# Optimization experiments

Hardware: AMD Instinct MI355X
Metric: run time of the kernel (lower is better)

The kernel has to match this reference:

```python
import jax, jax.numpy as jnp
import numpy as np

N_HEAD = 16
N_KV_HEAD = 4
D_HEAD = 128
RMS_EPS = 1.1920929e-07  # torch default eps for fp32 rms_norm


def _rms_norm(x):
    return x * jax.lax.rsqrt(jnp.mean(x * x, axis=-1, keepdims=True) + RMS_EPS)


def _rotary_tables(n_pos, dim):
    # dim = d_head; freq table has dim//2 entries (half of them zero)
    angular_freq = (1.0 / 1024.0) ** jnp.linspace(0.0, 1.0, dim // 4, dtype=jnp.float32)
    angular_freq = jnp.concatenate([angular_freq, jnp.zeros(dim // 4, jnp.float32)])
    theta = jnp.arange(n_pos, dtype=jnp.float32)[:, None] * angular_freq[None, :]
    return jnp.cos(theta), jnp.sin(theta)


def _apply_rotary(x):
    # x: (B, H, T, D). Faithful to source: cos/sin indexed by x.shape[-3] (= H),
    # broadcast over the time axis.
    n = x.shape[-3]
    cos, sin = _rotary_tables(n, x.shape[-1])
    cos = cos[None, :, None, :]
    sin = sin[None, :, None, :]
    xf = x.astype(jnp.float32)
    x1, x2 = jnp.split(xf, 2, axis=-1)
    y1 = x1 * cos + x2 * sin
    y2 = -x1 * sin + x2 * cos
    return jnp.concatenate([y1, y2], axis=-1).astype(x.dtype)


def setup_inputs() -> dict:
    key = jax.random.key(0)
    k1, k2, k3, k4 = jax.random.split(key, 4)
    B, T, C = 2, 2048, 2048
    return {
        "x": jax.random.normal(k1, (B, T, C), jnp.float32),
        "Wq": jax.random.normal(k2, (C, C), jnp.float32) * 0.02,
        "Wkv": jax.random.normal(k3, (2 * N_KV_HEAD * D_HEAD, C), jnp.float32) * 0.02,
        "Wproj": jax.random.normal(k4, (C, C), jnp.float32) * 0.02,
        "tok_masks": jnp.ones((B, T), jnp.int32),
    }


def reference(x, Wq, Wkv, Wproj, tok_masks):
    B, T, C = x.shape
    nh, nkv, dh = N_HEAD, N_KV_HEAD, D_HEAD

    q = (x @ Wq.T).reshape(B, T, nh, dh).transpose(0, 2, 1, 3)          # (B,nh,T,dh)
    kv = x @ Wkv.T                                                       # (B,T,2*nkv*dh)
    k, v = jnp.split(kv, 2, axis=2)
    k = k.reshape(B, T, nkv, dh).transpose(0, 2, 1, 3)                   # (B,nkv,T,dh)
    v = v.reshape(B, T, nkv, dh).transpose(0, 2, 1, 3)

    q, k = _rms_norm(q), _rms_norm(k)
    q, k = _apply_rotary(q), _apply_rotary(k)

    # GQA: repeat kv heads to match query heads
    rep = nh // nkv
    k = jnp.repeat(k, rep, axis=1)
    v = jnp.repeat(v, rep, axis=1)

    scale = 1.0 / jnp.sqrt(jnp.float32(dh))
    scores = jnp.einsum("bhqd,bhkd->bhqk", q, k) * scale                 # (B,nh,T,T)
    causal = jnp.tril(jnp.ones((T, T), bool))
    scores = jnp.where(causal[None, None], scores, -jnp.inf)
    attn = jax.nn.softmax(scores, axis=-1)
    y = jnp.einsum("bhqk,bhkd->bhqd", attn, v)                           # (B,nh,T,dh)
    y = y.transpose(0, 2, 1, 3).reshape(B, T, C)
    y = y @ Wproj.T
    return (y, jnp.float32(0.0))
```

## Files before the change

kernel.cpp:

```cpp
#include <hip/hip_runtime.h>
#include <hip/hip_bf16.h>

#define T_SEQ 2048
#define BATCH 2
#define CDIM  2048
#define NH    16
#define NKV   4
#define DH    128

typedef __attribute__((ext_vector_type(8))) short bfrag;
typedef __attribute__((ext_vector_type(4))) short bhalf;
typedef __attribute__((ext_vector_type(4))) float ffrag;
typedef __hip_bfloat16 bf16;

__device__ __forceinline__ void gll16(const bf16* __restrict__ g, bf16* lds) {
    __builtin_amdgcn_global_load_lds((const __attribute__((address_space(1))) void*)g,
                                     (__attribute__((address_space(3))) void*)lds, 16, 0, 0);
}

__device__ __forceinline__ unsigned cvt_pk_bf16(float lo, float hi) {
    unsigned r;
    asm("v_cvt_pk_bf16_f32 %0, %1, %2" : "=v"(r) : "v"(lo), "v"(hi));
    return r;
}

struct bf16x4 { bf16 a, b, c, d; };
#define N4_X   (BATCH * T_SEQ * CDIM / 4)
#define N4_WQ  (CDIM * CDIM / 4)
#define N4_WKV (2 * NKV * DH * CDIM / 4)
#define N4_WP  (CDIM * CDIM / 4)
__global__ __launch_bounds__(256) void cast_all(
    const float* __restrict__ x, const float* __restrict__ wq,
    const float* __restrict__ wkv, const float* __restrict__ wp,
    bf16* __restrict__ xb, bf16* __restrict__ wqb, bf16* __restrict__ wkvb, bf16* __restrict__ wpb)
{
    int j = blockIdx.x * 256 + threadIdx.x;
    const float* s; bf16* d;
    if (j < N4_X) { s = x; d = xb; }
    else {
        j -= N4_X;
        if (j < N4_WQ) { s = wq; d = wqb; }
        else {
            j -= N4_WQ;
            if (j < N4_WKV) { s = wkv; d = wkvb; }
            else { j -= N4_WKV; if (j >= N4_WP) return; s = wp; d = wpb; }
        }
    }
    float4 f = ((const float4*)s)[j];
    bf16x4 o{__float2bfloat16(f.x), __float2bfloat16(f.y),
             __float2bfloat16(f.z), __float2bfloat16(f.w)};
    ((bf16x4*)d)[j] = o;
}

template<int MODE, int BN>
__device__ __forceinline__ void gemm_body(
    const bf16* __restrict__ A, const bf16* __restrict__ W, int m0, int n0,
    bf16* __restrict__ out0, bf16* __restrict__ out1, float* __restrict__ outf,
    bf16* __restrict__ sA, bf16* __restrict__ sB)
{
    constexpr int NG = BN / 32;

    const int lane = threadIdx.x & 63;
    const int w    = threadIdx.x >> 6;
    const int wm   = w >> 1, wn = w & 1;
    const int lr   = lane & 15, quad = lane >> 4;

    const int pr8  = lane >> 3;
    const int ls   = (lane & 7) ^ pr8;
    const int rloc = 2 * (w * 8 + pr8) + (ls >> 2);
    const int k0s  = (ls & 3) * 8;

    const bf16* Aj0 = A + (size_t)(m0 +      rloc) * CDIM + k0s;
    const bf16* Aj1 = A + (size_t)(m0 + 64 + rloc) * CDIM + k0s;
    const bf16* Bj0 = W + (size_t)(n0 +      rloc) * CDIM + k0s;
    const bf16* Bj1 = W + (size_t)(n0 + 64 + rloc) * CDIM + k0s;
    bf16* dA0 = sA +        w * 512;
    bf16* dA1 = sA + 2048 + w * 512;
    bf16* dB0 = sB +        w * 512;
    bf16* dB1 = sB + 2048 + w * 512;

    const int soff = ((((lr & 1) << 2) | quad) ^ ((lr >> 1) & 7)) << 3;

    ffrag acc[4][NG] = {};
    for (int kk = 0; kk < CDIM; kk += 32) {
        __syncthreads();
        gll16(Aj0 + kk, dA0);
        gll16(Aj1 + kk, dA1);
        gll16(Bj0 + kk, dB0);
        if constexpr (BN == 128) gll16(Bj1 + kk, dB1);
        __syncthreads();

        bfrag af[4], bg[NG];
        #pragma unroll
        for (int f = 0; f < 4; ++f)
            af[f] = *(const bfrag*)&sA[((f * 16 + wm * 8 + (lr >> 1)) << 6) + soff];
        #pragma unroll
        for (int g = 0; g < NG; ++g)
            bg[g] = *(const bfrag*)&sB[((g * 16 + wn * 8 + (lr >> 1)) << 6) + soff];
        #pragma unroll
        for (int f = 0; f < 4; ++f)
            #pragma unroll
            for (int g = 0; g < NG; ++g)
                acc[f][g] = __builtin_amdgcn_mfma_f32_16x16x32_bf16(af[f], bg[g], acc[f][g], 0, 0, 0);
    }

    #pragma unroll
    for (int f = 0; f < 4; ++f) {
        #pragma unroll
        for (int g = 0; g < NG; ++g) {
            #pragma unroll
            for (int i = 0; i < 4; ++i) {
                const int m = m0 + f * 32 + wm * 16 + quad * 4 + i;
                const int n = n0 + g * 32 + wn * 16 + lr;
                const float v = acc[f][g][i];
                if constexpr (MODE == 0) {
                    int b = m >> 11, t = m & (T_SEQ - 1);
                    int h = n >> 7, d = n & (DH - 1);
                    out0[(((size_t)(b * NH + h) * T_SEQ + t) << 7) + d] = __float2bfloat16(v);
                } else if constexpr (MODE == 1) {
                    int b = m >> 11, t = m & (T_SEQ - 1);
                    if (n < NKV * DH) {
                        int h = n >> 7, d = n & (DH - 1);
                        out0[(((size_t)(b * NKV + h) * T_SEQ + t) << 7) + d] = __float2bfloat16(v);
                    } else {
                        int n2 = n - NKV * DH;
                        int h = n2 >> 7, d = n2 & (DH - 1);
                        out1[(((size_t)(b * NKV + h) * DH + d) << 11) + t] = __float2bfloat16(v);
                    }
                } else {
                    outf[(size_t)m * CDIM + n] = v;
                }
            }
        }
    }
}

__global__ __launch_bounds__(256) void gemm_qkv(
    const bf16* __restrict__ A, const bf16* __restrict__ Wq, const bf16* __restrict__ Wkv,
    bf16* __restrict__ q, bf16* __restrict__ k, bf16* __restrict__ vt)
{
    __shared__ __align__(16) bf16 sA[64 * 64];
    __shared__ __align__(16) bf16 sB[64 * 64];
    if (blockIdx.y < 16)
        gemm_body<0, 128>(A, Wq, blockIdx.x * 128, blockIdx.y * 128, q, nullptr, nullptr, sA, sB);
    else
        gemm_body<1, 128>(A, Wkv, blockIdx.x * 128, (blockIdx.y - 16) * 128, k, vt, nullptr, sA, sB);
}

__global__ __launch_bounds__(256) void gemm_proj(
    const bf16* __restrict__ A, const bf16* __restrict__ W, float* __restrict__ outf)
{
    __shared__ __align__(16) bf16 sA[64 * 64];
    __shared__ __align__(16) bf16 sB[32 * 64];
    gemm_body<2, 64>(A, W, blockIdx.x * 128, blockIdx.y * 64, nullptr, nullptr, outf, sA, sB);
    if (blockIdx.x == 0 && blockIdx.y == 0 && threadIdx.x == 0)
        outf[(size_t)BATCH * T_SEQ * CDIM] = 0.0f;
}

#define QROWS (BATCH * NH * T_SEQ)
#define KROWS (BATCH * NKV * T_SEQ)
__global__ __launch_bounds__(256) void normrope_k(bf16* __restrict__ qb, bf16* __restrict__ kb) {
    int row = blockIdx.x * 4 + (threadIdx.x >> 6);
    bf16* bufb; int nheads;
    if (row < QROWS) { bufb = qb; nheads = NH; }
    else { row -= QROWS; bufb = kb; nheads = NKV; }
    const int h = (row >> 11) % nheads;
    bf16* p = bufb + (size_t)row * DH;
    const int d = threadIdx.x & 63;
    float x1 = __bfloat162float(p[d]);
    float x2 = __bfloat162float(p[d + 64]);
    float ss = x1 * x1 + x2 * x2;
    #pragma unroll
    for (int off = 32; off; off >>= 1) ss += __shfl_xor(ss, off);
    float r = rsqrtf(ss * (1.0f / 128.0f) + 1.1920929e-07f);
    x1 *= r; x2 *= r;
    float freq = (d < 32) ? exp2f(-10.0f * (float)d * (1.0f / 31.0f)) : 0.0f;
    float th = (float)h * freq;
    float c, s;
    __sincosf(th, &s, &c);
    p[d]      = __float2bfloat16(x1 * c + x2 * s);
    p[d + 64] = __float2bfloat16(-x1 * s + x2 * c);
}

__global__ __launch_bounds__(512, 2) void attn_k(const bf16* __restrict__ Q, const bf16* __restrict__ K,
                                                 const bf16* __restrict__ VT, bf16* __restrict__ Y)
{
    const int lane = threadIdx.x & 63;
    const int w = threadIdx.x >> 6;
    const int g = w >> 2, wl = w & 3;
    const int h = blockIdx.y, b = blockIdx.z;
    const int lr = lane & 15, quad = lane >> 4, lk = quad * 8;
    const bf16* Qb = Q  + (size_t)(b * NH  + h)        * T_SEQ * DH;
    const bf16* Kb = K  + (size_t)(b * NKV + (h >> 2)) * T_SEQ * DH;
    const bf16* Vb = VT + (size_t)(b * NKV + (h >> 2)) * DH * T_SEQ;

    __shared__ __align__(16) union ShmU {
        struct { bf16 SK[2][2][32 * 128]; bf16 SV[2][2][128 * 32]; } s;
        ffrag MRG[9 * 4 * 64];
    } shm;

    const int k_r0 = wl * 8 + (lane >> 4);
    const int k_ch = lane & 15;
    const int v_r0 = wl * 32 + (lane >> 2);
    const int v_ch = lane & 3;
    const int vsw = (lr + (lr >> 2)) & 3;
    const float scale = 0.08838834764831845f;

    auto load_v_perm = [&](const bf16* rp) {
        union { bhalf h[2]; bfrag f; } u;
        u.h[0] = *(const bhalf*)(rp + v_ch * 4);
        u.h[1] = *(const bhalf*)(rp + 16 + v_ch * 4);
        return u.f;
    };

    const int qb = 15 - blockIdx.x;
    const int nc = 2 * (qb + 1);
    const int q0 = qb * 128 + wl * 32;

    bfrag qf[2][4];
    #pragma unroll
    for (int t = 0; t < 2; ++t)
        #pragma unroll
        for (int dc = 0; dc < 4; ++dc)
            qf[t][dc] = *(const bfrag*)(Qb + (size_t)(q0 + t * 16 + lr) * DH + dc * 32 + lk);

    float lp[2] = {};
    ffrag o[2][8] = {};

    bfrag kr[2], vr[2];
    {
        const int b0 = g * 32;
        #pragma unroll
        for (int j = 0; j < 2; ++j) {
            kr[j] = *(const bfrag*)(Kb + (size_t)(b0 + k_r0 + j * 4) * DH + k_ch * 8);
            vr[j] = load_v_perm(Vb + (size_t)(v_r0 + j * 16) * T_SEQ + b0);
        }
        #pragma unroll
        for (int j = 0; j < 2; ++j) {
            int krow = k_r0 + j * 4;
            *(bfrag*)&shm.s.SK[g][0][krow * 128 + ((k_ch ^ (krow & 15))) * 8] = kr[j];
            int vrow = v_r0 + j * 16;
            *(bfrag*)&shm.s.SV[g][0][vrow * 32 + ((v_ch ^ ((vrow + (vrow >> 2)) & 3))) * 8] = vr[j];
        }
        if (nc > 1) {
            const int nb = 64 + g * 32;
            #pragma unroll
            for (int j = 0; j < 2; ++j) {
                kr[j] = *(const bfrag*)(Kb + (size_t)(nb + k_r0 + j * 4) * DH + k_ch * 8);
                vr[j] = load_v_perm(Vb + (size_t)(v_r0 + j * 16) * T_SEQ + nb);
            }
        }
    }
    __syncthreads();

    for (int c = 0; c < nc; ++c) {
        const int cur = c & 1, nxt = cur ^ 1;
        const int base = c * 64 + g * 32;
        const bf16* SKc = shm.s.SK[g][cur];
        const bf16* SVc = shm.s.SV[g][cur];

        if (c + 1 < nc) {
            #pragma unroll
            for (int j = 0; j < 2; ++j) {
                int krow = k_r0 + j * 4;
                *(bfrag*)&shm.s.SK[g][nxt][krow * 128 + ((k_ch ^ (krow & 15))) * 8] = kr[j];
                int vrow = v_r0 + j * 16;
                *(bfrag*)&shm.s.SV[g][nxt][vrow * 32 + ((v_ch ^ ((vrow + (vrow >> 2)) & 3))) * 8] = vr[j];
            }
            if (c + 2 < nc) {
                const int nb = (c + 2) * 64 + g * 32;
                #pragma unroll
                for (int j = 0; j < 2; ++j) {
                    kr[j] = *(const bfrag*)(Kb + (size_t)(nb + k_r0 + j * 4) * DH + k_ch * 8);
                    vr[j] = load_v_perm(Vb + (size_t)(v_r0 + j * 16) * T_SEQ + nb);
                }
            }
        }

        ffrag s2[2][2] = {};
        #pragma unroll
        for (int kt = 0; kt < 2; ++kt)
            #pragma unroll
            for (int dc = 0; dc < 4; ++dc) {
                bfrag kf = *(const bfrag*)&SKc[(kt * 16 + lr) * 128 + (((dc << 2) | quad) ^ lr) * 8];
                s2[0][kt] = __builtin_amdgcn_mfma_f32_16x16x32_bf16(kf, qf[0][dc], s2[0][kt], 0, 0, 0);
                s2[1][kt] = __builtin_amdgcn_mfma_f32_16x16x32_bf16(kf, qf[1][dc], s2[1][kt], 0, 0, 0);
            }

        const bool maskc = (c >= 2 * qb);
        bfrag pf[2];
        #pragma unroll
        for (int t = 0; t < 2; ++t) {
            const int qa = q0 + t * 16 + lr;
            float ev[2][4];
            #pragma unroll
            for (int kt = 0; kt < 2; ++kt)
                #pragma unroll
                for (int i = 0; i < 4; ++i) {
                    const int ka = base + kt * 16 + quad * 4 + i;
                    float e = (!maskc || ka <= qa) ? __expf(fmaf(s2[t][kt][i], scale, -16.0f)) : 0.0f;
                    lp[t] += e;
                    ev[kt][i] = e;
                }
            union { unsigned u[4]; bfrag f; } pu;
            pu.u[0] = cvt_pk_bf16(ev[0][0], ev[0][1]);
            pu.u[1] = cvt_pk_bf16(ev[0][2], ev[0][3]);
            pu.u[2] = cvt_pk_bf16(ev[1][0], ev[1][1]);
            pu.u[3] = cvt_pk_bf16(ev[1][2], ev[1][3]);
            pf[t] = pu.f;
        }

        #pragma unroll
        for (int dt = 0; dt < 8; ++dt) {
            bfrag vf = *(const bfrag*)&SVc[(dt * 16 + lr) * 32 + ((quad ^ vsw)) * 8];
            o[0][dt] = __builtin_amdgcn_mfma_f32_16x16x32_bf16(pf[0], vf, o[0][dt], 0, 0, 0);
            o[1][dt] = __builtin_amdgcn_mfma_f32_16x16x32_bf16(pf[1], vf, o[1][dt], 0, 0, 0);
        }

        __syncthreads();
    }

    __syncthreads();
    #pragma unroll
    for (int t = 0; t < 2; ++t) {
        if (g == 1) {
            #pragma unroll
            for (int d = 0; d < 8; ++d) shm.MRG[(d * 4 + wl) * 64 + lane] = o[t][d];
            ffrag l4 = {lp[t], 0.0f, 0.0f, 0.0f};
            shm.MRG[(8 * 4 + wl) * 64 + lane] = l4;
        }
        __syncthreads();
        if (g == 0) {
            #pragma unroll
            for (int d = 0; d < 8; ++d) o[t][d] += shm.MRG[(d * 4 + wl) * 64 + lane];
            float lsum = lp[t] + shm.MRG[(8 * 4 + wl) * 64 + lane][0];
            lsum += __shfl_xor(lsum, 16);
            lsum += __shfl_xor(lsum, 32);
            float inv[4];
            #pragma unroll
            for (int i = 0; i < 4; ++i)
                inv[i] = 1.0f / __shfl(lsum, quad * 4 + i);
            #pragma unroll
            for (int dt = 0; dt < 8; ++dt)
                #pragma unroll
                for (int i = 0; i < 4; ++i) {
                    int row = q0 + t * 16 + quad * 4 + i;
                    Y[((size_t)(b * T_SEQ) + row) * CDIM + h * DH + dt * 16 + lr] =
                        __float2bfloat16(o[t][dt][i] * inv[i]);
                }
        }
        __syncthreads();
    }
}

extern "C" void kernel_launch(void* const* d_in, const int* in_sizes, int n_in,
                              void* d_out, int out_size, void* d_ws, size_t ws_size,
                              hipStream_t stream) {
    const float* x     = (const float*)d_in[0];
    const float* Wq    = (const float*)d_in[1];
    const float* Wkv   = (const float*)d_in[2];
    const float* Wproj = (const float*)d_in[3];
    float* out = (float*)d_out;

    char* ws = (char*)d_ws;
    size_t off = 0;
    auto alloc = [&](size_t bytes) { void* p = ws + off; off += (bytes + 255) & ~255ULL; return p; };
    bf16* xb   = (bf16*)alloc((size_t)BATCH * T_SEQ * CDIM * 2);
    bf16* wqb  = (bf16*)alloc((size_t)CDIM * CDIM * 2);
    bf16* wkvb = (bf16*)alloc((size_t)2 * NKV * DH * CDIM * 2);
    bf16* wpb  = (bf16*)alloc((size_t)CDIM * CDIM * 2);
    bf16* qb   = (bf16*)alloc((size_t)BATCH * NH * T_SEQ * DH * 2);
    bf16* kb   = (bf16*)alloc((size_t)BATCH * NKV * T_SEQ * DH * 2);
    bf16* vtb  = (bf16*)alloc((size_t)BATCH * NKV * DH * T_SEQ * 2);
    bf16* y1   = (bf16*)alloc((size_t)BATCH * T_SEQ * CDIM * 2);

    const int total4 = N4_X + N4_WQ + N4_WKV + N4_WP;
    cast_all<<<(total4 + 255) / 256, 256, 0, stream>>>(x, Wq, Wkv, Wproj, xb, wqb, wkvb, wpb);

    gemm_qkv<<<dim3(32, 24), 256, 0, stream>>>(xb, wqb, wkvb, qb, kb, vtb);
    normrope_k<<<(QROWS + KROWS) / 4, 256, 0, stream>>>(qb, kb);
    attn_k<<<dim3(16, NH, BATCH), 512, 0, stream>>>(qb, kb, vtb, y1);
    gemm_proj<<<dim3(32, 32), 256, 0, stream>>>(y1, wpb, out);
}
```

Baseline: 340.6 us.

## Restructure attention into 4-wave blocks with paired causal query tiles

The attention kernel goes from 512-thread blocks, where two wave groups split the key range and merge partial results through shared memory, to 256-thread blocks. Each wave now owns 16 query rows and sweeps all keys in 64-key chunks. Each block handles two query tiles (p and 15-p) in sequence so causal work is balanced across blocks. This removes the cross-group merge and its barriers, but halves the waves per block and makes each block's work serial over two passes.

```diff
diff --git a/kernel.cpp b/kernel.cpp
--- a/kernel.cpp
+++ b/kernel.cpp
@@ -182,174 +182,157 @@
     p[d + 64] = __float2bfloat16(-x1 * s + x2 * c);
 }
 
-__global__ __launch_bounds__(512, 2) void attn_k(const bf16* __restrict__ Q, const bf16* __restrict__ K,
+__global__ __launch_bounds__(256, 2) void attn_k(const bf16* __restrict__ Q, const bf16* __restrict__ K,
                                                  const bf16* __restrict__ VT, bf16* __restrict__ Y)
 {
     const int lane = threadIdx.x & 63;
     const int w = threadIdx.x >> 6;
-    const int g = w >> 2, wl = w & 3;
+    const int p = blockIdx.x >> 1, half = blockIdx.x & 1;
     const int h = blockIdx.y, b = blockIdx.z;
     const int lr = lane & 15, quad = lane >> 4, lk = quad * 8;
     const bf16* Qb = Q  + (size_t)(b * NH  + h)        * T_SEQ * DH;
     const bf16* Kb = K  + (size_t)(b * NKV + (h >> 2)) * T_SEQ * DH;
     const bf16* Vb = VT + (size_t)(b * NKV + (h >> 2)) * DH * T_SEQ;
 
-    __shared__ __align__(16) union ShmU {
-        struct { bf16 SK[2][2][32 * 128]; bf16 SV[2][2][128 * 32]; } s;
-        ffrag MRG[9 * 4 * 64];
-    } shm;
-
-    const int k_r0 = wl * 8 + (lane >> 4);
-    const int k_ch = lane & 15;
-    const int v_r0 = wl * 32 + (lane >> 2);
-    const int v_ch = lane & 3;
-    const int vsw = (lr + (lr >> 2)) & 3;
+    __shared__ __align__(16) bf16 SK[2][64 * 128];
+    __shared__ __align__(16) bf16 SV[2][128 * 64];
+
+    const int k_row = w * 16 + quad;
+    const int k_ch  = lane & 15;
+    const int v_row = w * 32 + (lane >> 3);
+    const int v_sl  = lane & 7;
+    const int vc    = v_sl ^ (lane >> 3);
+    const int vH    = vc >> 2, vs = vc & 3;
     const float scale = 0.08838834764831845f;
 
-    auto load_v_perm = [&](const bf16* rp) {
-        union { bhalf h[2]; bfrag f; } u;
-        u.h[0] = *(const bhalf*)(rp + v_ch * 4);
-        u.h[1] = *(const bhalf*)(rp + 16 + v_ch * 4);
+    auto load_v = [&](int kbase, int j) {
+        const bf16* rp = Vb + (size_t)(v_row + j * 8) * T_SEQ + kbase;
+        union { bhalf h2[2]; bfrag f; } u;
+        u.h2[0] = *(const bhalf*)(rp + vH * 32 + vs * 4);
+        u.h2[1] = *(const bhalf*)(rp + vH * 32 + 16 + vs * 4);
         return u.f;
     };
 
-    const int qb = 15 - blockIdx.x;
-    const int nc = 2 * (qb + 1);
-    const int q0 = qb * 128 + wl * 32;
-
-    bfrag qf[2][4];
-    #pragma unroll
-    for (int t = 0; t < 2; ++t)
+    for (int pass = 0; pass < 2; ++pass) {
+        const int qb = pass ? (15 - p) : p;
+        const int nc = 2 * (qb + 1);
+        const int q0w = qb * 128 + half * 64 + w * 16;
+
+        bfrag qf[4];
         #pragma unroll
         for (int dc = 0; dc < 4; ++dc)
-            qf[t][dc] = *(const bfrag*)(Qb + (size_t)(q0 + t * 16 + lr) * DH + dc * 32 + lk);
-
-    float lp[2] = {};
-    ffrag o[2][8] = {};
-
-    bfrag kr[2], vr[2];
-    {
-        const int b0 = g * 32;
-        #pragma unroll
-        for (int j = 0; j < 2; ++j) {
-            kr[j] = *(const bfrag*)(Kb + (size_t)(b0 + k_r0 + j * 4) * DH + k_ch * 8);
-            vr[j] = load_v_perm(Vb + (size_t)(v_r0 + j * 16) * T_SEQ + b0);
-        }
-        #pragma unroll
-        for (int j = 0; j < 2; ++j) {
-            int krow = k_r0 + j * 4;
-            *(bfrag*)&shm.s.SK[g][0][krow * 128 + ((k_ch ^ (krow & 15))) * 8] = kr[j];
-            int vrow = v_r0 + j * 16;
-            *(bfrag*)&shm.s.SV[g][0][vrow * 32 + ((v_ch ^ ((vrow + (vrow >> 2)) & 3))) * 8] = vr[j];
-        }
-        if (nc > 1) {
-            const int nb = 64 + g * 32;
-            #pragma unroll
-            for (int j = 0; j < 2; ++j) {
-                kr[j] = *(const bfrag*)(Kb + (size_t)(nb + k_r0 + j * 4) * DH + k_ch * 8);
-                vr[j] = load_v_perm(Vb + (size_t)(v_r0 + j * 16) * T_SEQ + nb);
-            }
-        }
-    }
-    __syncthreads();
-
-    for (int c = 0; c < nc; ++c) {
-        const int cur = c & 1, nxt = cur ^ 1;
-        const int base = c * 64 + g * 32;
-        const bf16* SKc = shm.s.SK[g][cur];
-        const bf16* SVc = shm.s.SV[g][cur];
-
-        if (c + 1 < nc) {
-            #pragma unroll
-            for (int j = 0; j < 2; ++j) {
-                int krow = k_r0 + j * 4;
-                *(bfrag*)&shm.s.SK[g][nxt][krow * 128 + ((k_ch ^ (krow & 15))) * 8] = kr[j];
-                int vrow = v_r0 + j * 16;
-                *(bfrag*)&shm.s.SV[g][nxt][vrow * 32 + ((v_ch ^ ((vrow + (vrow >> 2)) & 3))) * 8] = vr[j];
-            }
-            if (c + 2 < nc) {
-                const int nb = (c + 2) * 64 + g * 32;
+            qf[dc] = *(const bfrag*)(Qb + (size_t)(q0w + lr) * DH + dc * 32 + lk);
+
+        float lp = 0.0f;
+        ffrag o[8] = {};
+
+        bfrag kr[4], vr[4];
+        #pragma unroll
+        for (int j = 0; j < 4; ++j) {
+            kr[j] = *(const bfrag*)(Kb + (size_t)(k_row + j * 4) * DH + k_ch * 8);
+            vr[j] = load_v(0, j);
+        }
+        #pragma unroll
+        for (int j = 0; j < 4; ++j) {
+            int krow = k_row + j * 4;
+            *(bfrag*)&SK[0][krow * 128 + ((k_ch ^ (krow & 15)) << 3)] = kr[j];
+            int vrow = v_row + j * 8;
+            *(bfrag*)&SV[0][vrow * 64 + (v_sl << 3)] = vr[j];
+        }
+        #pragma unroll
+        for (int j = 0; j < 4; ++j) {
+            kr[j] = *(const bfrag*)(Kb + (size_t)(64 + k_row + j * 4) * DH + k_ch * 8);
+            vr[j] = load_v(64, j);
+        }
+        __syncthreads();
+
+        for (int c = 0; c < nc; ++c) {
+            const int cur = c & 1, nxt = cur ^ 1;
+            const int base = c * 64;
+            const bf16* SKc = SK[cur];
+            const bf16* SVc = SV[cur];
+
+            if (c + 1 < nc) {
                 #pragma unroll
-                for (int j = 0; j < 2; ++j) {
-                    kr[j] = *(const bfrag*)(Kb + (size_t)(nb + k_r0 + j * 4) * DH + k_ch * 8);
-                    vr[j] = load_v_perm(Vb + (size_t)(v_r0 + j * 16) * T_SEQ + nb);
-                }
-            }
-        }
-
-        ffrag s2[2][2] = {};
-        #pragma unroll
-        for (int kt = 0; kt < 2; ++kt)
-            #pragma unroll
-            for (int dc = 0; dc < 4; ++dc) {
-                bfrag kf = *(const bfrag*)&SKc[(kt * 16 + lr) * 128 + (((dc << 2) | quad) ^ lr) * 8];
-                s2[0][kt] = __builtin_amdgcn_mfma_f32_16x16x32_bf16(kf, qf[0][dc], s2[0][kt], 0, 0, 0);
-                s2[1][kt] = __builtin_amdgcn_mfma_f32_16x16x32_bf16(kf, qf[1][dc], s2[1][kt], 0, 0, 0);
-            }
-
-        const bool maskc = (c >= 2 * qb);
-        bfrag pf[2];
-        #pragma unroll
-        for (int t = 0; t < 2; ++t) {
-            const int qa = q0 + t * 16 + lr;
-            float ev[2][4];
-            #pragma unroll
-            for (int kt = 0; kt < 2; ++kt)
+                for (int j = 0; j < 4; ++j) {
+                    int krow = k_row + j * 4;
+                    *(bfrag*)&SK[nxt][krow * 128 + ((k_ch ^ (krow & 15)) << 3)] = kr[j];
+                    int vrow = v_row + j * 8;
+                    *(bfrag*)&SV[nxt][vrow * 64 + (v_sl << 3)] = vr[j];
+                }
+                if (c + 2 < nc) {
+                    const int nb = (c + 2) * 64;
+                    #pragma unroll
+                    for (int j = 0; j < 4; ++j) {
+                        kr[j] = *(const bfrag*)(Kb + (size_t)(nb + k_row + j * 4) * DH + k_ch * 8);
+                        vr[j] = load_v(nb, j);
+                    }
+                }
+            }
+
+            ffrag s2[4] = {};
+            #pragma unroll
+            for (int kt = 0; kt < 4; ++kt)
+                #pragma unroll
+                for (int dc = 0; dc < 4; ++dc) {
+                    bfrag kf = *(const bfrag*)&SKc[(kt * 16 + lr) * 128 + ((((dc << 2) | quad) ^ lr) << 3)];
+                    s2[kt] = __builtin_amdgcn_mfma_f32_16x16x32_bf16(kf, qf[dc], s2[kt], 0, 0, 0);
+                }
+
+            const bool maskc = (c >= 2 * qb);
+            const int qa = q0w + lr;
+            float ev[4][4];
+            #pragma unroll
+            for (int kt = 0; kt < 4; ++kt)
                 #pragma unroll
                 for (int i = 0; i < 4; ++i) {
                     const int ka = base + kt * 16 + quad * 4 + i;
-                    float e = (!maskc || ka <= qa) ? __expf(fmaf(s2[t][kt][i], scale, -16.0f)) : 0.0f;
-                    lp[t] += e;
+                    float e = (!maskc || ka <= qa) ? __expf(fmaf(s2[kt][i], scale, -16.0f)) : 0.0f;
+                    lp += e;
                     ev[kt][i] = e;
                 }
-            union { unsigned u[4]; bfrag f; } pu;
-            pu.u[0] = cvt_pk_bf16(ev[0][0], ev[0][1]);
-            pu.u[1] = cvt_pk_bf16(ev[0][2], ev[0][3]);
-            pu.u[2] = cvt_pk_bf16(ev[1][0], ev[1][1]);
-            pu.u[3] = cvt_pk_bf16(ev[1][2], ev[1][3]);
-            pf[t] = pu.f;
-        }
-
-        #pragma unroll
-        for (int dt = 0; dt < 8; ++dt) {
-            bfrag vf = *(const bfrag*)&SVc[(dt * 16 + lr) * 32 + ((quad ^ vsw)) * 8];
-            o[0][dt] = __builtin_amdgcn_mfma_f32_16x16x32_bf16(pf[0], vf, o[0][dt], 0, 0, 0);
-            o[1][dt] = __builtin_amdgcn_mfma_f32_16x16x32_bf16(pf[1], vf, o[1][dt], 0, 0, 0);
-        }
-
-        __syncthreads();
-    }
-
-    __syncthreads();
-    #pragma unroll
-    for (int t = 0; t < 2; ++t) {
-        if (g == 1) {
-            #pragma unroll
-            for (int d = 0; d < 8; ++d) shm.MRG[(d * 4 + wl) * 64 + lane] = o[t][d];
-            ffrag l4 = {lp[t], 0.0f, 0.0f, 0.0f};
-            shm.MRG[(8 * 4 + wl) * 64 + lane] = l4;
-        }
-        __syncthreads();
-        if (g == 0) {
-            #pragma unroll
-            for (int d = 0; d < 8; ++d) o[t][d] += shm.MRG[(d * 4 + wl) * 64 + lane];
-            float lsum = lp[t] + shm.MRG[(8 * 4 + wl) * 64 + lane][0];
-            lsum += __shfl_xor(lsum, 16);
-            lsum += __shfl_xor(lsum, 32);
-            float inv[4];
-            #pragma unroll
-            for (int i = 0; i < 4; ++i)
-                inv[i] = 1.0f / __shfl(lsum, quad * 4 + i);
-            #pragma unroll
-            for (int dt = 0; dt < 8; ++dt)
-                #pragma unroll
-                for (int i = 0; i < 4; ++i) {
-                    int row = q0 + t * 16 + quad * 4 + i;
-                    Y[((size_t)(b * T_SEQ) + row) * CDIM + h * DH + dt * 16 + lr] =
-                        __float2bfloat16(o[t][dt][i] * inv[i]);
-                }
-        }
-        __syncthreads();
+            bfrag pf[2];
+            {
+                union { unsigned u[4]; bfrag f; } pu;
+                pu.u[0] = cvt_pk_bf16(ev[0][0], ev[0][1]);
+                pu.u[1] = cvt_pk_bf16(ev[0][2], ev[0][3]);
+                pu.u[2] = cvt_pk_bf16(ev[1][0], ev[1][1]);
+                pu.u[3] = cvt_pk_bf16(ev[1][2], ev[1][3]);
+                pf[0] = pu.f;
+                pu.u[0] = cvt_pk_bf16(ev[2][0], ev[2][1]);
+                pu.u[1] = cvt_pk_bf16(ev[2][2], ev[2][3]);
+                pu.u[2] = cvt_pk_bf16(ev[3][0], ev[3][1]);
+                pu.u[3] = cvt_pk_bf16(ev[3][2], ev[3][3]);
+                pf[1] = pu.f;
+            }
+
+            #pragma unroll
+            for (int dt = 0; dt < 8; ++dt) {
+                const int vrow = dt * 16 + lr;
+                bfrag vf0 = *(const bfrag*)&SVc[vrow * 64 + ((quad ^ (lr & 7)) << 3)];
+                bfrag vf1 = *(const bfrag*)&SVc[vrow * 64 + (((4 | quad) ^ (lr & 7)) << 3)];
+                o[dt] = __builtin_amdgcn_mfma_f32_16x16x32_bf16(pf[0], vf0, o[dt], 0, 0, 0);
+                o[dt] = __builtin_amdgcn_mfma_f32_16x16x32_bf16(pf[1], vf1, o[dt], 0, 0, 0);
+            }
+
+            __syncthreads();
+        }
+
+        float lsum = lp;
+        lsum += __shfl_xor(lsum, 16);
+        lsum += __shfl_xor(lsum, 32);
+        float inv[4];
+        #pragma unroll
+        for (int i = 0; i < 4; ++i)
+            inv[i] = 1.0f / __shfl(lsum, quad * 4 + i);
+        #pragma unroll
+        for (int dt = 0; dt < 8; ++dt)
+            #pragma unroll
+            for (int i = 0; i < 4; ++i) {
+                int row = q0w + quad * 4 + i;
+                Y[((size_t)(b * T_SEQ) + row) * CDIM + h * DH + dt * 16 + lr] =
+                    __float2bfloat16(o[dt][i] * inv[i]);
+            }
     }
 }
 
@@ -379,6 +362,6 @@
 
     gemm_qkv<<<dim3(32, 24), 256, 0, stream>>>(xb, wqb, wkvb, qb, kb, vtb);
     normrope_k<<<(QROWS + KROWS) / 4, 256, 0, stream>>>(qb, kb);
-    attn_k<<<dim3(16, NH, BATCH), 512, 0, stream>>>(qb, kb, vtb, y1);
+    attn_k<<<dim3(16, NH, BATCH), 256, 0, stream>>>(qb, kb, vtb, y1);
     gemm_proj<<<dim3(32, 32), 256, 0, stream>>>(y1, wpb, out);
 }
```

New measurement: 303.6 us. 10.9% less time.
